# Optimization experiments

Hardware: AMD Instinct MI355X
Metric: run time of the kernel (lower is better)

Reference implementation:

```python
import jax, jax.numpy as jnp
import numpy as np

B, LQ, LK, DK, DV = 16, 1024, 1024, 256, 256
NEG = -1e9


def setup_inputs() -> dict:
    key = jax.random.key(0)
    kq, kk, kv, kw, km = jax.random.split(key, 5)
    return {
        "query": jax.random.normal(kq, (B, LQ, DK), dtype=jnp.float32),
        "key": jax.random.normal(kk, (B, LK, DK), dtype=jnp.float32),
        "value": jax.random.normal(kv, (B, LK, DV), dtype=jnp.float32),
        "w": jax.random.normal(kw, (DK,), dtype=jnp.float32),  # Linear(d_k,1,bias=False) weight
        "mask": jax.random.randint(km, (B, LQ, LK), 0, 2, dtype=jnp.int32),
    }


def reference(query, key, value, w, mask):
    # Bahdanau additive score: alignment_layer(query[:, :, None] + key[:, None, :]).squeeze(-1)
    # Exact linear decomposition: W·(q+k) = W·q + W·k, avoiding the (Lq,Lk,d_k) intermediate.
    q_s = jnp.einsum("bqd,d->bq", query, w)  # [B, Lq]
    k_s = jnp.einsum("bkd,d->bk", key, w)    # [B, Lk]
    scores = q_s[:, :, None] + k_s[:, None, :]  # [B, Lq, Lk]
    scores = jnp.where(mask == 0, NEG, scores)
    p_attn = jax.nn.softmax(scores, axis=-1)
    return jnp.matmul(p_attn, value)  # [B, Lq, Dv]
```

## Files before the change

### kernel.cpp

```cpp
#include <hip/hip_runtime.h>
#include <math.h>


#define NB     16
#define NL     1024
#define ND     256
#define NBKT   128

__global__ __launch_bounds__(256)
void ks_kernel(const float* __restrict__ key, const float* __restrict__ w,
               float* __restrict__ ks) {
    int wid  = threadIdx.x >> 6;
    int lane = threadIdx.x & 63;
    int row  = blockIdx.x * 4 + wid;
    const float4* krow = (const float4*)(key + (size_t)row * ND);
    float4 kv = krow[lane];
    float4 wv = ((const float4*)w)[lane];
    float p = kv.x * wv.x + kv.y * wv.y + kv.z * wv.z + kv.w * wv.w;
    #pragma unroll
    for (int off = 32; off > 0; off >>= 1)
        p += __shfl_xor(p, off, 64);
    if (lane == 0) ks[row] = p;
}

__global__ __launch_bounds__(1024)
void select_kernel(const float* __restrict__ ks,
                   float2* __restrict__ pk, float* __restrict__ rem) {
    __shared__ float red[NL];
    __shared__ float se[NL];
    __shared__ int   cnt[NBKT];
    __shared__ int   cur[NBKT];
    __shared__ float csum[16];
    const int b = blockIdx.x;
    const int t = threadIdx.x;
    const int lane = t & 63;
    const int wid  = t >> 6;

    float v = ks[b * NL + t];

    red[t] = v;
    __syncthreads();
    for (int off = 512; off > 0; off >>= 1) {
        if (t < off) red[t] = fmaxf(red[t], red[t + off]);
        __syncthreads();
    }
    const float m = red[0];
    __syncthreads();

    const float e = __expf(v - m);

    if (t < NBKT) cnt[t] = 0;
    __syncthreads();
    int bkt = (int)fminf(m - v, (float)(NBKT - 1));
    atomicAdd(&cnt[bkt], 1);
    __syncthreads();

    if (t < NBKT) cur[t] = cnt[t];
    __syncthreads();
    for (int off = 1; off < NBKT; off <<= 1) {
        int add = 0;
        if (t < NBKT && t >= off) add = cur[t - off];
        __syncthreads();
        if (t < NBKT) cur[t] += add;
        __syncthreads();
    }
    if (t < NBKT) cur[t] -= cnt[t];
    __syncthreads();

    int p = atomicAdd(&cur[bkt], 1);
    se[p] = e;
    pk[b * NL + p] = make_float2(e, __int_as_float(t));
    __syncthreads();

    float s = se[wid * 64 + lane];
    #pragma unroll
    for (int off = 32; off > 0; off >>= 1)
        s += __shfl_xor(s, off, 64);
    if (lane == 0) csum[wid] = s;
    __syncthreads();

    if (t == 0) {
        float run = 0.0f;
        for (int c = 15; c >= 0; --c) {
            rem[b * NL + c * 64 + 63] = run;
            run += csum[c];
        }
    }
}

__global__ __launch_bounds__(256)
void attn_kernel(const float* __restrict__ value, const int* __restrict__ mask,
                 const float2* __restrict__ pk, const float* __restrict__ rem,
                 float* __restrict__ out) {
    const int wid  = threadIdx.x >> 6;
    const int lane = threadIdx.x & 63;
    const int row  = blockIdx.x * 4 + wid;
    const int b    = row >> 10;
    const int base = b << 10;

    const float4*  vbase = (const float4*)(value + ((size_t)b << 10) * ND);
    const float2*  pk_g  = pk + base;

    const int4* mrow4 = (const int4*)(mask + (size_t)row * NL);
    unsigned int bits = 0;
    #pragma unroll
    for (int j = 0; j < 4; ++j) {
        int4 m = mrow4[lane * 4 + j];
        bits |= (m.x != 0 ? 1u : 0u) << (j * 4 + 0);
        bits |= (m.y != 0 ? 1u : 0u) << (j * 4 + 1);
        bits |= (m.z != 0 ? 1u : 0u) << (j * 4 + 2);
        bits |= (m.w != 0 ? 1u : 0u) << (j * 4 + 3);
    }

    float4 acc = make_float4(0.f, 0.f, 0.f, 0.f);
    float Z = 0.0f;
    bool done = false;

    for (int c = 0; c < 16 && !done; ++c) {
        float2 p = pk_g[c * 64 + lane];
        float e  = p.x;
        int   k  = __float_as_int(p.y);

        unsigned int bk = (unsigned int)
            __builtin_amdgcn_ds_bpermute((k >> 4) << 2, (int)bits);
        bool mb = (bk >> (k & 15)) & 1u;

        unsigned long long bm = __ballot(mb);
        int NA = __popcll(bm);

        float em = mb ? e : 0.0f;
        #pragma unroll
        for (int off = 32; off > 0; off >>= 1)
            em += __shfl_xor(em, off, 64);
        Z += em;

        if (NA > 0) {
            unsigned int lo = (unsigned int)bm, hi = (unsigned int)(bm >> 32);
            int cntA = __builtin_amdgcn_mbcnt_hi(hi,
                       __builtin_amdgcn_mbcnt_lo(lo, 0));
            int dest = mb ? cntA : (NA + (lane - cntA));
            int ec = __builtin_amdgcn_ds_permute(dest << 2, __float_as_int(e));
            int kc = __builtin_amdgcn_ds_permute(dest << 2, k);

            #pragma unroll 4
            for (int i = 0; i < NA; ++i) {
                float es  = __int_as_float(__builtin_amdgcn_readlane(ec, i));
                int   ksv = __builtin_amdgcn_readlane(kc, i);
                float4 v  = vbase[(size_t)ksv * 64 + lane];
                acc.x += es * v.x; acc.y += es * v.y;
                acc.z += es * v.z; acc.w += es * v.w;
            }
        }
        done = (rem[base + c * 64 + 63] <= 1e-5f * Z);
    }

    float4* orow = (float4*)(out + (size_t)row * ND);
    if (Z > 0.0f) {
        float inv = 1.0f / Z;
        orow[lane] = make_float4(acc.x * inv, acc.y * inv, acc.z * inv, acc.w * inv);
    } else {
        float4 s = make_float4(0.f, 0.f, 0.f, 0.f);
        for (int k = 0; k < NL; ++k) {
            float4 v = vbase[(size_t)k * 64 + lane];
            s.x += v.x; s.y += v.y; s.z += v.z; s.w += v.w;
        }
        const float inv = 1.0f / (float)NL;
        orow[lane] = make_float4(s.x * inv, s.y * inv, s.z * inv, s.w * inv);
    }
}

extern "C" void kernel_launch(void* const* d_in, const int* in_sizes, int n_in,
                              void* d_out, int out_size, void* d_ws, size_t ws_size,
                              hipStream_t stream) {
    const float* key   = (const float*)d_in[1];
    const float* value = (const float*)d_in[2];
    const float* w     = (const float*)d_in[3];
    const int*   mask  = (const int*)d_in[4];
    float*       outp  = (float*)d_out;

    float*  ks  = (float*)d_ws;
    float2* pkb = (float2*)(ks + NB * NL);
    float*  rem = (float*)(pkb + NB * NL);

    ks_kernel    <<<NB * NL / 4, 256, 0, stream>>>(key, w, ks);
    select_kernel<<<NB, 1024, 0, stream>>>(ks, pkb, rem);
    attn_kernel  <<<NB * NL / 4, 256, 0, stream>>>(value, mask, pkb, rem, outp);
}
```

Before: 175.8 us.

## Stage first-chunk value rows in LDS shared by 16 query rows per block

Attention blocks grow to 16 waves, each handling one query row. The 64 value rows of the first sorted-key chunk are loaded cooperatively into 64 KB of LDS and reused by all 16 rows. The first chunk's accumulation reads from LDS and uses four independent accumulators to expose ILP, and Z is summed inside the loops instead of by a wave reduction. The large LDS footprint and 1024-thread blocks limit occupancy, and every block now pays the staging cost and a barrier.

```diff
diff --git a/kernel.cpp b/kernel.cpp
--- a/kernel.cpp
+++ b/kernel.cpp
@@ -88,18 +88,31 @@
     }
 }
 
-__global__ __launch_bounds__(256)
+__global__ __launch_bounds__(1024)
 void attn_kernel(const float* __restrict__ value, const int* __restrict__ mask,
                  const float2* __restrict__ pk, const float* __restrict__ rem,
                  float* __restrict__ out) {
+    __shared__ float lds_V[64 * ND];
+
     const int wid  = threadIdx.x >> 6;
     const int lane = threadIdx.x & 63;
-    const int row  = blockIdx.x * 4 + wid;
+    const int row  = blockIdx.x * 16 + wid;
     const int b    = row >> 10;
     const int base = b << 10;
 
-    const float4*  vbase = (const float4*)(value + ((size_t)b << 10) * ND);
-    const float2*  pk_g  = pk + base;
+    const float4* vbase = (const float4*)(value + ((size_t)b << 10) * ND);
+    const float2* pk_g  = pk + base;
+
+    float2 p0 = pk_g[lane];
+    float e0 = p0.x;
+    int   k0 = __float_as_int(p0.y);
+
+    #pragma unroll
+    for (int j = 0; j < 4; ++j) {
+        int s  = wid * 4 + j;
+        int ks = __builtin_amdgcn_readlane(k0, s);
+        ((float4*)lds_V)[s * 64 + lane] = vbase[(size_t)ks * 64 + lane];
+    }
 
     const int4* mrow4 = (const int4*)(mask + (size_t)row * NL);
     unsigned int bits = 0;
@@ -112,41 +125,82 @@
         bits |= (m.w != 0 ? 1u : 0u) << (j * 4 + 3);
     }
 
-    float4 acc = make_float4(0.f, 0.f, 0.f, 0.f);
+    __syncthreads();
+
+    unsigned int bk = (unsigned int)
+        __builtin_amdgcn_ds_bpermute((k0 >> 4) << 2, (int)bits);
+    bool mb = (bk >> (k0 & 15)) & 1u;
+    unsigned long long bm = __ballot(mb);
+    int NA = __popcll(bm);
+    unsigned int blo = (unsigned int)bm, bhi = (unsigned int)(bm >> 32);
+    int cntA = __builtin_amdgcn_mbcnt_hi(bhi,
+               __builtin_amdgcn_mbcnt_lo(blo, 0));
+    int dest = mb ? cntA : (NA + (lane - cntA));
+    int ec = __builtin_amdgcn_ds_permute(dest << 2, __float_as_int(e0));
+    int sc = __builtin_amdgcn_ds_permute(dest << 2, lane);
+
+    float4 a0 = make_float4(0.f, 0.f, 0.f, 0.f);
+    float4 a1 = make_float4(0.f, 0.f, 0.f, 0.f);
+    float4 a2 = make_float4(0.f, 0.f, 0.f, 0.f);
+    float4 a3 = make_float4(0.f, 0.f, 0.f, 0.f);
     float Z = 0.0f;
-    bool done = false;
-
-    for (int c = 0; c < 16 && !done; ++c) {
+
+    int i = 0;
+    for (; i + 4 <= NA; i += 4) {
+        int   s0 = __builtin_amdgcn_readlane(sc, i);
+        int   s1 = __builtin_amdgcn_readlane(sc, i + 1);
+        int   s2 = __builtin_amdgcn_readlane(sc, i + 2);
+        int   s3 = __builtin_amdgcn_readlane(sc, i + 3);
+        float w0 = __int_as_float(__builtin_amdgcn_readlane(ec, i));
+        float w1 = __int_as_float(__builtin_amdgcn_readlane(ec, i + 1));
+        float w2 = __int_as_float(__builtin_amdgcn_readlane(ec, i + 2));
+        float w3 = __int_as_float(__builtin_amdgcn_readlane(ec, i + 3));
+        float4 v0 = ((const float4*)lds_V)[s0 * 64 + lane];
+        float4 v1 = ((const float4*)lds_V)[s1 * 64 + lane];
+        float4 v2 = ((const float4*)lds_V)[s2 * 64 + lane];
+        float4 v3 = ((const float4*)lds_V)[s3 * 64 + lane];
+        Z += w0 + w1 + w2 + w3;
+        a0.x += w0 * v0.x; a0.y += w0 * v0.y; a0.z += w0 * v0.z; a0.w += w0 * v0.w;
+        a1.x += w1 * v1.x; a1.y += w1 * v1.y; a1.z += w1 * v1.z; a1.w += w1 * v1.w;
+        a2.x += w2 * v2.x; a2.y += w2 * v2.y; a2.z += w2 * v2.z; a2.w += w2 * v2.w;
+        a3.x += w3 * v3.x; a3.y += w3 * v3.y; a3.z += w3 * v3.z; a3.w += w3 * v3.w;
+    }
+    for (; i < NA; ++i) {
+        int   s0 = __builtin_amdgcn_readlane(sc, i);
+        float w0 = __int_as_float(__builtin_amdgcn_readlane(ec, i));
+        float4 v0 = ((const float4*)lds_V)[s0 * 64 + lane];
+        Z += w0;
+        a0.x += w0 * v0.x; a0.y += w0 * v0.y; a0.z += w0 * v0.z; a0.w += w0 * v0.w;
+    }
+
+    float4 acc = make_float4(a0.x + a1.x + a2.x + a3.x,
+                             a0.y + a1.y + a2.y + a3.y,
+                             a0.z + a1.z + a2.z + a3.z,
+                             a0.w + a1.w + a2.w + a3.w);
+    bool done = (rem[base + 63] <= 1e-5f * Z);
+
+    for (int c = 1; c < 16 && !done; ++c) {
         float2 p = pk_g[c * 64 + lane];
         float e  = p.x;
         int   k  = __float_as_int(p.y);
-
-        unsigned int bk = (unsigned int)
+        unsigned int bk2 = (unsigned int)
             __builtin_amdgcn_ds_bpermute((k >> 4) << 2, (int)bits);
-        bool mb = (bk >> (k & 15)) & 1u;
-
-        unsigned long long bm = __ballot(mb);
-        int NA = __popcll(bm);
-
-        float em = mb ? e : 0.0f;
-        #pragma unroll
-        for (int off = 32; off > 0; off >>= 1)
-            em += __shfl_xor(em, off, 64);
-        Z += em;
-
-        if (NA > 0) {
-            unsigned int lo = (unsigned int)bm, hi = (unsigned int)(bm >> 32);
-            int cntA = __builtin_amdgcn_mbcnt_hi(hi,
-                       __builtin_amdgcn_mbcnt_lo(lo, 0));
-            int dest = mb ? cntA : (NA + (lane - cntA));
-            int ec = __builtin_amdgcn_ds_permute(dest << 2, __float_as_int(e));
-            int kc = __builtin_amdgcn_ds_permute(dest << 2, k);
-
+        bool mb2 = (bk2 >> (k & 15)) & 1u;
+        unsigned long long bm2 = __ballot(mb2);
+        int NA2 = __popcll(bm2);
+        if (NA2 > 0) {
+            unsigned int lo2 = (unsigned int)bm2, hi2 = (unsigned int)(bm2 >> 32);
+            int cnt2 = __builtin_amdgcn_mbcnt_hi(hi2,
+                       __builtin_amdgcn_mbcnt_lo(lo2, 0));
+            int d2 = mb2 ? cnt2 : (NA2 + (lane - cnt2));
+            int ec2 = __builtin_amdgcn_ds_permute(d2 << 2, __float_as_int(e));
+            int kc2 = __builtin_amdgcn_ds_permute(d2 << 2, k);
             #pragma unroll 4
-            for (int i = 0; i < NA; ++i) {
-                float es  = __int_as_float(__builtin_amdgcn_readlane(ec, i));
-                int   ksv = __builtin_amdgcn_readlane(kc, i);
+            for (int t = 0; t < NA2; ++t) {
+                float es  = __int_as_float(__builtin_amdgcn_readlane(ec2, t));
+                int   ksv = __builtin_amdgcn_readlane(kc2, t);
                 float4 v  = vbase[(size_t)ksv * 64 + lane];
+                Z += es;
                 acc.x += es * v.x; acc.y += es * v.y;
                 acc.z += es * v.z; acc.w += es * v.w;
             }
@@ -184,5 +238,5 @@
 
     ks_kernel    <<<NB * NL / 4, 256, 0, stream>>>(key, w, ks);
     select_kernel<<<NB, 1024, 0, stream>>>(ks, pkb, rem);
-    attn_kernel  <<<NB * NL / 4, 256, 0, stream>>>(value, mask, pkb, rem, outp);
-}
+    attn_kernel  <<<NB * NL / 16, 1024, 0, stream>>>(value, mask, pkb, rem, outp);
+}
```

Measured after the change: 166.5 us. 1.06x faster.
